# Kernel tuning notes

Hardware: AMD Instinct MI355X
Metric: run time of the kernel (lower is better)

The kernel has to match this reference:

```python
import math
import jax, jax.numpy as jnp
import numpy as np

B, T, C = 4, 2048, 1024
NH = 16
HD = C // NH  # 64

def setup_inputs() -> dict:
    key = jax.random.key(0)
    k1, k2, k3 = jax.random.split(key, 3)
    x = jax.random.normal(k1, (B, T, C), dtype=jnp.float32)
    # init scale ~ 1/sqrt(fan_in) to keep activations sane
    W_attn = jax.random.normal(k2, (C, 3 * C), dtype=jnp.float32) * (1.0 / math.sqrt(C))
    b_attn = jnp.zeros((3 * C,), dtype=jnp.float32)
    W_proj = jax.random.normal(k3, (C, C), dtype=jnp.float32) * (1.0 / math.sqrt(C))
    b_proj = jnp.zeros((C,), dtype=jnp.float32)
    return {"x": x, "W_attn": W_attn, "b_attn": b_attn, "W_proj": W_proj, "b_proj": b_proj}

def reference(x, W_attn, b_attn, W_proj, b_proj):
    b, t, c = x.shape
    qkv = x @ W_attn + b_attn                      # [B,T,3C]
    q, k, v = jnp.split(qkv, 3, axis=-1)           # each [B,T,C]
    # [B,T,C] -> [B,NH,T,HD]
    def heads(z):
        return z.reshape(b, t, NH, HD).transpose(0, 2, 1, 3)
    q, k, v = heads(q), heads(k), heads(v)
    scale = 1.0 / math.sqrt(HD)
    att = jnp.einsum('bhqd,bhkd->bhqk', q, k) * scale   # [B,NH,T,T]
    causal = jnp.tril(jnp.ones((t, t), dtype=bool))      # [T,T]
    att = jnp.where(causal[None, None, :, :], att, -jnp.inf)
    att = jax.nn.softmax(att, axis=-1)
    # dropout p=0.0 -> identity
    y = jnp.einsum('bhqk,bhkd->bhqd', att, v)            # [B,NH,T,HD]
    y = y.transpose(0, 2, 1, 3).reshape(b, t, c)         # [B,T,C]
    return y @ W_proj + b_proj
```

## Files before the change

### kernel.cpp

```cpp
#include <hip/hip_runtime.h>
#include <hip/hip_bf16.h>


typedef __bf16 bf16;
typedef __bf16 bf16x4 __attribute__((ext_vector_type(4)));
typedef __bf16 bf16x8 __attribute__((ext_vector_type(8)));
typedef float  f32x4  __attribute__((ext_vector_type(4)));

#define MFMA16(a, b, c) __builtin_amdgcn_mfma_f32_16x16x32_bf16((a), (b), (c), 0, 0, 0)

#define GLOAD16(g, l)                                                 \
    __builtin_amdgcn_global_load_lds(                                 \
        (const __attribute__((address_space(1))) void*)(g),           \
        (__attribute__((address_space(3))) void*)(l), 16, 0, 0)

static constexpr int Bsz = 4;
static constexpr int T   = 2048;
static constexpr int Cc  = 1024;
static constexpr int NH  = 16;
static constexpr int HD  = 64;
static constexpr int C3  = 3 * Cc;

__global__ void prep(const float* __restrict__ x, bf16* __restrict__ xb,
                     const float* __restrict__ W_attn, bf16* __restrict__ WtA) {
    const int bid = blockIdx.x;
    const int tid = threadIdx.x;
    if (bid < 4096) {
        size_t i = ((size_t)bid * 256 + tid) * 8;
        f32x4 a0 = *(const f32x4*)(x + i);
        f32x4 a1 = *(const f32x4*)(x + i + 4);
        bf16x8 v;
#pragma unroll
        for (int e = 0; e < 4; ++e) { v[e] = (bf16)a0[e]; v[e + 4] = (bf16)a1[e]; }
        *(bf16x8*)(xb + i) = v;
    } else {
        __shared__ float tile[32][33];
        const int tb = bid - 4096;
        const int bx = (tb % (C3 / 32)) * 32;
        const int by = (tb / (C3 / 32)) * 32;
        const int tx = tid & 31, ty = tid >> 5;
#pragma unroll
        for (int i = 0; i < 32; i += 8)
            tile[ty + i][tx] = W_attn[(size_t)(by + ty + i) * C3 + bx + tx];
        __syncthreads();
#pragma unroll
        for (int i = 0; i < 32; i += 8)
            WtA[(size_t)(bx + ty + i) * Cc + by + tx] = (bf16)tile[tx][ty + i];
    }
}

__global__ void transpose_f32_bf16(const float* __restrict__ in, bf16* __restrict__ out,
                                   int R, int Ccols) {
    __shared__ float tile[32][33];
    int bx = blockIdx.x * 32;
    int by = blockIdx.y * 32;
    int tx = threadIdx.x, ty = threadIdx.y;
#pragma unroll
    for (int i = 0; i < 32; i += 8)
        tile[ty + i][tx] = in[(size_t)(by + ty + i) * Ccols + bx + tx];
    __syncthreads();
#pragma unroll
    for (int i = 0; i < 32; i += 8)
        out[(size_t)(bx + ty + i) * R + by + tx] = (bf16)tile[tx][ty + i];
}

__global__ __launch_bounds__(256)
void gemm_qkv(const bf16* __restrict__ A, const bf16* __restrict__ Bt,
              const float* __restrict__ bias,
              bf16* __restrict__ qo, bf16* __restrict__ ko, bf16* __restrict__ vt,
              int M, int N, int K) {
    constexpr int BM = 128, BN = 128, BK = 64;
    __shared__ bf16 As[2][BM * BK];
    __shared__ bf16 Bs[2][BN * BK];

    const int tid  = threadIdx.x;
    const int wave = tid >> 6, lane = tid & 63;
    const int quad = lane >> 4, l16 = lane & 15;
    const int wm = wave & 1, wn = wave >> 1;
    const int m0 = blockIdx.x * BM, n0 = blockIdx.y * BN;

    f32x4 acc[4][4] = {};

    const int lrow = lane >> 3;
    const int lcol = (lane & 7) * 8;
    const bf16* Ab = A  + (size_t)(m0 + wave * 8 + lrow) * K + lcol;
    const bf16* Bb = Bt + (size_t)(n0 + wave * 8 + lrow) * K + lcol;
    const int wofs = wave * 512;

#pragma unroll
    for (int r = 0; r < 4; ++r) {
        GLOAD16(Ab + (size_t)r * 32 * K, As[0] + wofs + r * 2048);
        GLOAD16(Bb + (size_t)r * 32 * K, Bs[0] + wofs + r * 2048);
    }

    int cur = 0;
    for (int k0 = 0; k0 < K; k0 += BK) {
        __syncthreads();
        if (k0 + BK < K) {
#pragma unroll
            for (int r = 0; r < 4; ++r) {
                GLOAD16(Ab + (size_t)r * 32 * K + k0 + BK, As[cur ^ 1] + wofs + r * 2048);
                GLOAD16(Bb + (size_t)r * 32 * K + k0 + BK, Bs[cur ^ 1] + wofs + r * 2048);
            }
        }
        const bf16* Asc = As[cur];
        const bf16* Bsc = Bs[cur];
#pragma unroll
        for (int ks = 0; ks < 2; ++ks) {
            bf16x8 af[4], bfr[4];
#pragma unroll
            for (int i = 0; i < 4; ++i)
                af[i] = *(const bf16x8*)(&Asc[(wm * 64 + i * 16 + l16) * BK + ks * 32 + quad * 8]);
#pragma unroll
            for (int j = 0; j < 4; ++j)
                bfr[j] = *(const bf16x8*)(&Bsc[(wn * 64 + j * 16 + l16) * BK + ks * 32 + quad * 8]);
#pragma unroll
            for (int i = 0; i < 4; ++i)
#pragma unroll
                for (int j = 0; j < 4; ++j)
                    acc[i][j] = MFMA16(af[i], bfr[j], acc[i][j]);
        }
        cur ^= 1;
    }

    const int which = n0 >> 10;
    const int nc0 = n0 & 1023;
    if (which < 2) {
        bf16* dst = which ? ko : qo;
#pragma unroll
        for (int j = 0; j < 4; ++j) {
            int colg = n0 + wn * 64 + j * 16 + l16;
            int coll = nc0 + wn * 64 + j * 16 + l16;
            float bv = bias[colg];
#pragma unroll
            for (int i = 0; i < 4; ++i) {
                int rowb = m0 + wm * 64 + i * 16 + quad * 4;
#pragma unroll
                for (int r = 0; r < 4; ++r)
                    dst[(size_t)(rowb + r) * Cc + coll] = (bf16)(acc[i][j][r] + bv);
            }
        }
    } else {
#pragma unroll
        for (int j = 0; j < 4; ++j) {
            int colg = n0 + wn * 64 + j * 16 + l16;
            int coll = nc0 + wn * 64 + j * 16 + l16;
            int h = coll >> 6, d = coll & 63;
            float bv = bias[colg];
            bf16* vhead_d = vt + ((size_t)h * HD + d) * T;
#pragma unroll
            for (int i = 0; i < 4; ++i) {
                int rowb = m0 + wm * 64 + i * 16 + quad * 4;
                int b = rowb >> 11;
                int t = rowb & 2047;
                bf16x4 pk;
#pragma unroll
                for (int r = 0; r < 4; ++r) pk[r] = (bf16)(acc[i][j][r] + bv);
                *(bf16x4*)(vhead_d + (size_t)b * NH * HD * T + t) = pk;
            }
        }
    }
}

__global__ __launch_bounds__(256)
void gemm_bt(const bf16* __restrict__ A, const bf16* __restrict__ Bt,
             const float* __restrict__ bias, float* __restrict__ C,
             int M, int N, int K) {
    constexpr int BM = 128, BN = 128, BK = 64;
    __shared__ bf16 As[2][BM * BK];
    __shared__ bf16 Bs[2][BN * BK];

    const int tid  = threadIdx.x;
    const int wave = tid >> 6, lane = tid & 63;
    const int quad = lane >> 4, l16 = lane & 15;
    const int wm = wave & 1, wn = wave >> 1;
    const int m0 = blockIdx.x * BM, n0 = blockIdx.y * BN;

    f32x4 acc[4][4] = {};

    const int lrow = lane >> 3;
    const int lcol = (lane & 7) * 8;
    const bf16* Ab = A  + (size_t)(m0 + wave * 8 + lrow) * K + lcol;
    const bf16* Bb = Bt + (size_t)(n0 + wave * 8 + lrow) * K + lcol;
    const int wofs = wave * 512;

#pragma unroll
    for (int r = 0; r < 4; ++r) {
        GLOAD16(Ab + (size_t)r * 32 * K, As[0] + wofs + r * 2048);
        GLOAD16(Bb + (size_t)r * 32 * K, Bs[0] + wofs + r * 2048);
    }

    int cur = 0;
    for (int k0 = 0; k0 < K; k0 += BK) {
        __syncthreads();
        if (k0 + BK < K) {
#pragma unroll
            for (int r = 0; r < 4; ++r) {
                GLOAD16(Ab + (size_t)r * 32 * K + k0 + BK, As[cur ^ 1] + wofs + r * 2048);
                GLOAD16(Bb + (size_t)r * 32 * K + k0 + BK, Bs[cur ^ 1] + wofs + r * 2048);
            }
        }
        const bf16* Asc = As[cur];
        const bf16* Bsc = Bs[cur];
#pragma unroll
        for (int ks = 0; ks < 2; ++ks) {
            bf16x8 af[4], bfr[4];
#pragma unroll
            for (int i = 0; i < 4; ++i)
                af[i] = *(const bf16x8*)(&Asc[(wm * 64 + i * 16 + l16) * BK + ks * 32 + quad * 8]);
#pragma unroll
            for (int j = 0; j < 4; ++j)
                bfr[j] = *(const bf16x8*)(&Bsc[(wn * 64 + j * 16 + l16) * BK + ks * 32 + quad * 8]);
#pragma unroll
            for (int i = 0; i < 4; ++i)
#pragma unroll
                for (int j = 0; j < 4; ++j)
                    acc[i][j] = MFMA16(af[i], bfr[j], acc[i][j]);
        }
        cur ^= 1;
    }

#pragma unroll
    for (int j = 0; j < 4; ++j) {
        int col = n0 + wn * 64 + j * 16 + l16;
        float bv = bias[col];
#pragma unroll
        for (int i = 0; i < 4; ++i) {
            int rowb = m0 + wm * 64 + i * 16 + quad * 4;
#pragma unroll
            for (int r = 0; r < 4; ++r)
                C[(size_t)(rowb + r) * N + col] = acc[i][j][r] + bv;
        }
    }
}

__global__ __launch_bounds__(256, 4)
void attn_fused(const bf16* __restrict__ qb, const bf16* __restrict__ kb,
                const bf16* __restrict__ vtb, bf16* __restrict__ y) {
    constexpr int LKD = 72;
    constexpr int LVT = 40;
    constexpr int LPS = 40;
    constexpr int QT = T / 64;
    __shared__ bf16 Ks[2][32 * LKD];
    __shared__ bf16 Vt[2][64 * LVT];
    __shared__ bf16 Ps[4][16 * LPS];

    const int tid  = threadIdx.x;
    const int wave = tid >> 6, lane = tid & 63;
    const int quad = lane >> 4, l16 = lane & 15;
    const int bid = blockIdx.x;
    const int pr = bid >> 6;
    const int hb = bid & 63;
    const int b = hb >> 4, h = hb & 15;

    const bf16* qbase  = qb + (size_t)b * T * Cc + h * HD;
    const bf16* kbase  = kb + (size_t)b * T * Cc + h * HD;
    const bf16* vthead = vtb + (size_t)(b * NH + h) * HD * T;
    bf16* yrow = y + (size_t)b * T * Cc + h * HD;

    const int srK = tid >> 3, scK = (tid & 7) * 8;
    const int srV = tid >> 2, scV = (tid & 3) * 8;

    bf16x8 ones;
#pragma unroll
    for (int e = 0; e < 8; ++e) ones[e] = (bf16)1.0f;

#pragma unroll 1
    for (int seg = 0; seg < 2; ++seg) {
        const int qt = (seg == 0) ? (QT - 1 - pr) : pr;
        const int q0 = qt * 64;

        bf16x8 qf[2];
        {
            int qrow = q0 + wave * 16 + l16;
#pragma unroll
            for (int dblk = 0; dblk < 2; ++dblk) {
                bf16x8 v = *(const bf16x8*)(qbase + (size_t)qrow * Cc + dblk * 32 + quad * 8);
#pragma unroll
                for (int e = 0; e < 8; ++e) v[e] = (bf16)((float)v[e] * 0.18033688f);
                qf[dblk] = v;
            }
        }

        f32x4 o[4] = {};
        f32x4 osum = {};

        const int w0 = q0 + wave * 16;
        const int nt = q0 / 32 + 2;

        bf16x8 kp = *(const bf16x8*)(kbase + (size_t)srK * Cc + scK);
        bf16x8 vp = *(const bf16x8*)(vthead + (size_t)srV * T + scV);
        __syncthreads();
        *(bf16x8*)(&Ks[0][srK * LKD + scK]) = kp;
        *(bf16x8*)(&Vt[0][srV * LVT + scV]) = vp;

        int cur = 0;
        for (int it = 0; it < nt; ++it) {
            const int kt = it * 32;
            __syncthreads();

            const bool more = (it + 1 < nt);
            if (more) {
                int ktn = kt + 32;
                kp = *(const bf16x8*)(kbase + (size_t)(ktn + srK) * Cc + scK);
                vp = *(const bf16x8*)(vthead + (size_t)srV * T + ktn + scV);
            }

            const bf16* ksc = Ks[cur];
            const bf16* vtc = Vt[cur];
            if (kt <= w0 + 15) {
                __builtin_amdgcn_s_setprio(1);
                f32x4 st[2] = {};
#pragma unroll
                for (int km = 0; km < 2; ++km) {
                    bf16x8 kf0 = *(const bf16x8*)(&ksc[(km * 16 + l16) * LKD + quad * 8]);
                    bf16x8 kf1 = *(const bf16x8*)(&ksc[(km * 16 + l16) * LKD + 32 + quad * 8]);
                    st[km] = MFMA16(kf0, qf[0], st[km]);
                    st[km] = MFMA16(kf1, qf[1], st[km]);
                }

                const bool needmask = (kt + 31 > w0);
                const int qrel = w0 + l16 - kt;
#pragma unroll
                for (int km = 0; km < 2; ++km)
#pragma unroll
                    for (int r = 0; r < 4; ++r) {
                        float v = st[km][r];
                        if (needmask) {
                            int key = km * 16 + quad * 4 + r;
                            v = (key <= qrel) ? v : -INFINITY;
                        }
                        st[km][r] = __builtin_exp2f(v);
                    }

                bf16* pw = &Ps[wave][0];
#pragma unroll
                for (int km = 0; km < 2; ++km) {
                    bf16x4 pk;
#pragma unroll
                    for (int r = 0; r < 4; ++r) pk[r] = (bf16)st[km][r];
                    *(bf16x4*)(&pw[l16 * LPS + km * 16 + quad * 4]) = pk;
                }
                bf16x8 pf = *(const bf16x8*)(&pw[l16 * LPS + quad * 8]);

#pragma unroll
                for (int dd = 0; dd < 4; ++dd) {
                    bf16x8 vf = *(const bf16x8*)(&vtc[(dd * 16 + l16) * LVT + quad * 8]);
                    o[dd] = MFMA16(pf, vf, o[dd]);
                }
                osum = MFMA16(pf, ones, osum);
                __builtin_amdgcn_s_setprio(0);
            }

            if (more) {
                *(bf16x8*)(&Ks[cur ^ 1][srK * LKD + scK]) = kp;
                *(bf16x8*)(&Vt[cur ^ 1][srV * LVT + scV]) = vp;
            }
            cur ^= 1;
        }

#pragma unroll
        for (int r = 0; r < 4; ++r) {
            float inv = 1.0f / osum[r];
            int t = w0 + quad * 4 + r;
#pragma unroll
            for (int dd = 0; dd < 4; ++dd)
                yrow[(size_t)t * Cc + dd * 16 + l16] = (bf16)(o[dd][r] * inv);
        }
    }
}

extern "C" void kernel_launch(void* const* d_in, const int* in_sizes, int n_in,
                              void* d_out, int out_size, void* d_ws, size_t ws_size,
                              hipStream_t stream) {
    const float* x      = (const float*)d_in[0];
    const float* W_attn = (const float*)d_in[1];
    const float* b_attn = (const float*)d_in[2];
    const float* W_proj = (const float*)d_in[3];
    const float* b_proj = (const float*)d_in[4];
    float* out = (float*)d_out;

    const int M = Bsz * T;
    const size_t R = (size_t)M * Cc;

    bf16* qb  = (bf16*)d_ws;
    bf16* kb  = qb + R;
    bf16* vtb = kb + R;
    bf16* xb  = vtb + R;
    bf16* yb  = xb;
    bf16* WtA = (bf16*)d_out;
    bf16* WtP = qb;

    prep<<<4096 + 3072, 256, 0, stream>>>(x, xb, W_attn, WtA);
    gemm_qkv<<<dim3(M / 128, C3 / 128), 256, 0, stream>>>(xb, WtA, b_attn, qb, kb, vtb, M, C3, Cc);
    attn_fused<<<1024, 256, 0, stream>>>(qb, kb, vtb, yb);
    transpose_f32_bf16<<<dim3(Cc / 32, Cc / 32), dim3(32, 8), 0, stream>>>(W_proj, WtP, Cc, Cc);
    gemm_bt<<<dim3(M / 128, Cc / 128), 256, 0, stream>>>(yb, WtP, b_proj, out, M, Cc, Cc);
}
```

Before: 274.4 us.

## Retile QKV GEMM to 256x128 with 512 threads and split attention into one tile per block

The QKV GEMM now uses 256x128 tiles with 8 waves and single-buffered LDS, synchronising after each load and each compute step instead of prefetching the next K-slice. This doubles the work per block and halves B-tile reloads, but gives up load/compute overlap inside a block. The attention kernel drops the paired short/long query-tile scheme: it launches 2048 blocks with one query tile each, longest tiles first, and raises the occupancy hint to 6. The goal is finer-grained scheduling and more resident waves, at the cost of relying on the hardware scheduler to balance the uneven causal tiles.

```diff
diff --git a/kernel.cpp b/kernel.cpp
--- a/kernel.cpp
+++ b/kernel.cpp
@@ -64,19 +64,19 @@
         out[(size_t)(bx + ty + i) * R + by + tx] = (bf16)tile[tx][ty + i];
 }
 
-__global__ __launch_bounds__(256)
+__global__ __launch_bounds__(512, 4)
 void gemm_qkv(const bf16* __restrict__ A, const bf16* __restrict__ Bt,
               const float* __restrict__ bias,
               bf16* __restrict__ qo, bf16* __restrict__ ko, bf16* __restrict__ vt,
               int M, int N, int K) {
-    constexpr int BM = 128, BN = 128, BK = 64;
-    __shared__ bf16 As[2][BM * BK];
-    __shared__ bf16 Bs[2][BN * BK];
+    constexpr int BM = 256, BN = 128, BK = 64;
+    __shared__ bf16 As[BM * BK];
+    __shared__ bf16 Bs[BN * BK];
 
     const int tid  = threadIdx.x;
     const int wave = tid >> 6, lane = tid & 63;
     const int quad = lane >> 4, l16 = lane & 15;
-    const int wm = wave & 1, wn = wave >> 1;
+    const int wm = wave >> 1, wn = wave & 1;
     const int m0 = blockIdx.x * BM, n0 = blockIdx.y * BN;
 
     f32x4 acc[4][4] = {};
@@ -87,40 +87,31 @@
     const bf16* Bb = Bt + (size_t)(n0 + wave * 8 + lrow) * K + lcol;
     const int wofs = wave * 512;
 
-#pragma unroll
-    for (int r = 0; r < 4; ++r) {
-        GLOAD16(Ab + (size_t)r * 32 * K, As[0] + wofs + r * 2048);
-        GLOAD16(Bb + (size_t)r * 32 * K, Bs[0] + wofs + r * 2048);
-    }
-
-    int cur = 0;
     for (int k0 = 0; k0 < K; k0 += BK) {
-        __syncthreads();
-        if (k0 + BK < K) {
-#pragma unroll
-            for (int r = 0; r < 4; ++r) {
-                GLOAD16(Ab + (size_t)r * 32 * K + k0 + BK, As[cur ^ 1] + wofs + r * 2048);
-                GLOAD16(Bb + (size_t)r * 32 * K + k0 + BK, Bs[cur ^ 1] + wofs + r * 2048);
-            }
-        }
-        const bf16* Asc = As[cur];
-        const bf16* Bsc = Bs[cur];
+#pragma unroll
+        for (int r = 0; r < 4; ++r)
+            GLOAD16(Ab + (size_t)(r * 64) * K + k0, As + wofs + r * 4096);
+#pragma unroll
+        for (int r = 0; r < 2; ++r)
+            GLOAD16(Bb + (size_t)(r * 64) * K + k0, Bs + wofs + r * 4096);
+        __syncthreads();
+
 #pragma unroll
         for (int ks = 0; ks < 2; ++ks) {
             bf16x8 af[4], bfr[4];
 #pragma unroll
             for (int i = 0; i < 4; ++i)
-                af[i] = *(const bf16x8*)(&Asc[(wm * 64 + i * 16 + l16) * BK + ks * 32 + quad * 8]);
+                af[i] = *(const bf16x8*)(&As[(wm * 64 + i * 16 + l16) * BK + ks * 32 + quad * 8]);
 #pragma unroll
             for (int j = 0; j < 4; ++j)
-                bfr[j] = *(const bf16x8*)(&Bsc[(wn * 64 + j * 16 + l16) * BK + ks * 32 + quad * 8]);
+                bfr[j] = *(const bf16x8*)(&Bs[(wn * 64 + j * 16 + l16) * BK + ks * 32 + quad * 8]);
 #pragma unroll
             for (int i = 0; i < 4; ++i)
 #pragma unroll
                 for (int j = 0; j < 4; ++j)
                     acc[i][j] = MFMA16(af[i], bfr[j], acc[i][j]);
         }
-        cur ^= 1;
+        __syncthreads();
     }
 
     const int which = n0 >> 10;
@@ -234,13 +225,12 @@
     }
 }
 
-__global__ __launch_bounds__(256, 4)
+__global__ __launch_bounds__(256, 6)
 void attn_fused(const bf16* __restrict__ qb, const bf16* __restrict__ kb,
                 const bf16* __restrict__ vtb, bf16* __restrict__ y) {
     constexpr int LKD = 72;
     constexpr int LVT = 40;
     constexpr int LPS = 40;
-    constexpr int QT = T / 64;
     __shared__ bf16 Ks[2][32 * LKD];
     __shared__ bf16 Vt[2][64 * LVT];
     __shared__ bf16 Ps[4][16 * LPS];
@@ -249,9 +239,10 @@
     const int wave = tid >> 6, lane = tid & 63;
     const int quad = lane >> 4, l16 = lane & 15;
     const int bid = blockIdx.x;
-    const int pr = bid >> 6;
+    const int qt = 31 - (bid >> 6);
     const int hb = bid & 63;
     const int b = hb >> 4, h = hb & 15;
+    const int q0 = qt * 64;
 
     const bf16* qbase  = qb + (size_t)b * T * Cc + h * HD;
     const bf16* kbase  = kb + (size_t)b * T * Cc + h * HD;
@@ -265,108 +256,101 @@
 #pragma unroll
     for (int e = 0; e < 8; ++e) ones[e] = (bf16)1.0f;
 
-#pragma unroll 1
-    for (int seg = 0; seg < 2; ++seg) {
-        const int qt = (seg == 0) ? (QT - 1 - pr) : pr;
-        const int q0 = qt * 64;
-
-        bf16x8 qf[2];
-        {
-            int qrow = q0 + wave * 16 + l16;
-#pragma unroll
-            for (int dblk = 0; dblk < 2; ++dblk) {
-                bf16x8 v = *(const bf16x8*)(qbase + (size_t)qrow * Cc + dblk * 32 + quad * 8);
-#pragma unroll
-                for (int e = 0; e < 8; ++e) v[e] = (bf16)((float)v[e] * 0.18033688f);
-                qf[dblk] = v;
-            }
-        }
-
-        f32x4 o[4] = {};
-        f32x4 osum = {};
-
-        const int w0 = q0 + wave * 16;
-        const int nt = q0 / 32 + 2;
-
-        bf16x8 kp = *(const bf16x8*)(kbase + (size_t)srK * Cc + scK);
-        bf16x8 vp = *(const bf16x8*)(vthead + (size_t)srV * T + scV);
-        __syncthreads();
-        *(bf16x8*)(&Ks[0][srK * LKD + scK]) = kp;
-        *(bf16x8*)(&Vt[0][srV * LVT + scV]) = vp;
-
-        int cur = 0;
-        for (int it = 0; it < nt; ++it) {
-            const int kt = it * 32;
-            __syncthreads();
-
-            const bool more = (it + 1 < nt);
-            if (more) {
-                int ktn = kt + 32;
-                kp = *(const bf16x8*)(kbase + (size_t)(ktn + srK) * Cc + scK);
-                vp = *(const bf16x8*)(vthead + (size_t)srV * T + ktn + scV);
-            }
-
-            const bf16* ksc = Ks[cur];
-            const bf16* vtc = Vt[cur];
-            if (kt <= w0 + 15) {
-                __builtin_amdgcn_s_setprio(1);
-                f32x4 st[2] = {};
-#pragma unroll
-                for (int km = 0; km < 2; ++km) {
-                    bf16x8 kf0 = *(const bf16x8*)(&ksc[(km * 16 + l16) * LKD + quad * 8]);
-                    bf16x8 kf1 = *(const bf16x8*)(&ksc[(km * 16 + l16) * LKD + 32 + quad * 8]);
-                    st[km] = MFMA16(kf0, qf[0], st[km]);
-                    st[km] = MFMA16(kf1, qf[1], st[km]);
+    bf16x8 qf[2];
+    {
+        int qrow = q0 + wave * 16 + l16;
+#pragma unroll
+        for (int dblk = 0; dblk < 2; ++dblk) {
+            bf16x8 v = *(const bf16x8*)(qbase + (size_t)qrow * Cc + dblk * 32 + quad * 8);
+#pragma unroll
+            for (int e = 0; e < 8; ++e) v[e] = (bf16)((float)v[e] * 0.18033688f);
+            qf[dblk] = v;
+        }
+    }
+
+    f32x4 o[4] = {};
+    f32x4 osum = {};
+
+    const int w0 = q0 + wave * 16;
+    const int nt = q0 / 32 + 2;
+
+    bf16x8 kp = *(const bf16x8*)(kbase + (size_t)srK * Cc + scK);
+    bf16x8 vp = *(const bf16x8*)(vthead + (size_t)srV * T + scV);
+    *(bf16x8*)(&Ks[0][srK * LKD + scK]) = kp;
+    *(bf16x8*)(&Vt[0][srV * LVT + scV]) = vp;
+
+    int cur = 0;
+    for (int it = 0; it < nt; ++it) {
+        const int kt = it * 32;
+        __syncthreads();
+
+        const bool more = (it + 1 < nt);
+        if (more) {
+            int ktn = kt + 32;
+            kp = *(const bf16x8*)(kbase + (size_t)(ktn + srK) * Cc + scK);
+            vp = *(const bf16x8*)(vthead + (size_t)srV * T + ktn + scV);
+        }
+
+        const bf16* ksc = Ks[cur];
+        const bf16* vtc = Vt[cur];
+        if (kt <= w0 + 15) {
+            __builtin_amdgcn_s_setprio(1);
+            f32x4 st[2] = {};
+#pragma unroll
+            for (int km = 0; km < 2; ++km) {
+                bf16x8 kf0 = *(const bf16x8*)(&ksc[(km * 16 + l16) * LKD + quad * 8]);
+                bf16x8 kf1 = *(const bf16x8*)(&ksc[(km * 16 + l16) * LKD + 32 + quad * 8]);
+                st[km] = MFMA16(kf0, qf[0], st[km]);
+                st[km] = MFMA16(kf1, qf[1], st[km]);
+            }
+
+            const bool needmask = (kt + 31 > w0);
+            const int qrel = w0 + l16 - kt;
+#pragma unroll
+            for (int km = 0; km < 2; ++km)
+#pragma unroll
+                for (int r = 0; r < 4; ++r) {
+                    float v = st[km][r];
+                    if (needmask) {
+                        int key = km * 16 + quad * 4 + r;
+                        v = (key <= qrel) ? v : -INFINITY;
+                    }
+                    st[km][r] = __builtin_exp2f(v);
                 }
 
-                const bool needmask = (kt + 31 > w0);
-                const int qrel = w0 + l16 - kt;
-#pragma unroll
-                for (int km = 0; km < 2; ++km)
-#pragma unroll
-                    for (int r = 0; r < 4; ++r) {
-                        float v = st[km][r];
-                        if (needmask) {
-                            int key = km * 16 + quad * 4 + r;
-                            v = (key <= qrel) ? v : -INFINITY;
-                        }
-                        st[km][r] = __builtin_exp2f(v);
-                    }
-
-                bf16* pw = &Ps[wave][0];
-#pragma unroll
-                for (int km = 0; km < 2; ++km) {
-                    bf16x4 pk;
-#pragma unroll
-                    for (int r = 0; r < 4; ++r) pk[r] = (bf16)st[km][r];
-                    *(bf16x4*)(&pw[l16 * LPS + km * 16 + quad * 4]) = pk;
-                }
-                bf16x8 pf = *(const bf16x8*)(&pw[l16 * LPS + quad * 8]);
-
-#pragma unroll
-                for (int dd = 0; dd < 4; ++dd) {
-                    bf16x8 vf = *(const bf16x8*)(&vtc[(dd * 16 + l16) * LVT + quad * 8]);
-                    o[dd] = MFMA16(pf, vf, o[dd]);
-                }
-                osum = MFMA16(pf, ones, osum);
-                __builtin_amdgcn_s_setprio(0);
-            }
-
-            if (more) {
-                *(bf16x8*)(&Ks[cur ^ 1][srK * LKD + scK]) = kp;
-                *(bf16x8*)(&Vt[cur ^ 1][srV * LVT + scV]) = vp;
-            }
-            cur ^= 1;
-        }
-
-#pragma unroll
-        for (int r = 0; r < 4; ++r) {
-            float inv = 1.0f / osum[r];
-            int t = w0 + quad * 4 + r;
-#pragma unroll
-            for (int dd = 0; dd < 4; ++dd)
-                yrow[(size_t)t * Cc + dd * 16 + l16] = (bf16)(o[dd][r] * inv);
-        }
+            bf16* pw = &Ps[wave][0];
+#pragma unroll
+            for (int km = 0; km < 2; ++km) {
+                bf16x4 pk;
+#pragma unroll
+                for (int r = 0; r < 4; ++r) pk[r] = (bf16)st[km][r];
+                *(bf16x4*)(&pw[l16 * LPS + km * 16 + quad * 4]) = pk;
+            }
+            bf16x8 pf = *(const bf16x8*)(&pw[l16 * LPS + quad * 8]);
+
+#pragma unroll
+            for (int dd = 0; dd < 4; ++dd) {
+                bf16x8 vf = *(const bf16x8*)(&vtc[(dd * 16 + l16) * LVT + quad * 8]);
+                o[dd] = MFMA16(pf, vf, o[dd]);
+            }
+            osum = MFMA16(pf, ones, osum);
+            __builtin_amdgcn_s_setprio(0);
+        }
+
+        if (more) {
+            *(bf16x8*)(&Ks[cur ^ 1][srK * LKD + scK]) = kp;
+            *(bf16x8*)(&Vt[cur ^ 1][srV * LVT + scV]) = vp;
+        }
+        cur ^= 1;
+    }
+
+#pragma unroll
+    for (int r = 0; r < 4; ++r) {
+        float inv = 1.0f / osum[r];
+        int t = w0 + quad * 4 + r;
+#pragma unroll
+        for (int dd = 0; dd < 4; ++dd)
+            yrow[(size_t)t * Cc + dd * 16 + l16] = (bf16)(o[dd][r] * inv);
     }
 }
 
@@ -392,8 +376,8 @@
     bf16* WtP = qb;
 
     prep<<<4096 + 3072, 256, 0, stream>>>(x, xb, W_attn, WtA);
-    gemm_qkv<<<dim3(M / 128, C3 / 128), 256, 0, stream>>>(xb, WtA, b_attn, qb, kb, vtb, M, C3, Cc);
-    attn_fused<<<1024, 256, 0, stream>>>(qb, kb, vtb, yb);
+    gemm_qkv<<<dim3(M / 256, C3 / 128), 512, 0, stream>>>(xb, WtA, b_attn, qb, kb, vtb, M, C3, Cc);
+    attn_fused<<<2048, 256, 0, stream>>>(qb, kb, vtb, yb);
     transpose_f32_bf16<<<dim3(Cc / 32, Cc / 32), dim3(32, 8), 0, stream>>>(W_proj, WtP, Cc, Cc);
     gemm_bt<<<dim3(M / 128, Cc / 128), 256, 0, stream>>>(yb, WtP, b_proj, out, M, Cc, Cc);
 }
```

Result: faster. 264.4 us (-3.6%).
